# Performance work log

Measured on AMD Instinct MI355X. Metric: run time of the kernel, lower is better.

Reference implementation:

```python
import jax, jax.numpy as jnp
import numpy as np

N = 50000      # nodes
E = 400000     # edges (avg degree 8)
F_IN = 128     # input feature dim
H = 4          # heads (layer 1)
D = 128        # hidden per head
C = 3          # classes (layer 2 out, 1 head)
EPS = 1e-5     # BatchNorm eps
SLOPE = 0.2    # LeakyReLU negative slope (DGL GATConv default)


def setup_inputs() -> dict:
    key = jax.random.key(0)
    ks = jax.random.split(key, 16)
    s = jnp.float32(0.05)
    return {
        "features": jax.random.normal(ks[0], (N, F_IN), jnp.float32),
        "src": jax.random.randint(ks[1], (E,), 0, N, jnp.int32),
        "dst": jax.random.randint(ks[2], (E,), 0, N, jnp.int32),
        # GATConv layer 1 params
        "W1": jax.random.normal(ks[3], (F_IN, H * D), jnp.float32) * s,
        "al1": jax.random.normal(ks[4], (H, D), jnp.float32) * s,
        "ar1": jax.random.normal(ks[5], (H, D), jnp.float32) * s,
        "b1": jnp.zeros((H * D,), jnp.float32),
        "Wres1": jax.random.normal(ks[6], (F_IN, H * D), jnp.float32) * s,
        # BatchNorm1d (inference mode)
        "bn_gamma": jnp.ones((H * D,), jnp.float32),
        "bn_beta": jnp.zeros((H * D,), jnp.float32),
        "bn_mean": jnp.zeros((H * D,), jnp.float32),
        "bn_var": jnp.ones((H * D,), jnp.float32),
        # GATConv layer 2 params (1 head, C out)
        "W2": jax.random.normal(ks[7], (H * D, C), jnp.float32) * s,
        "al2": jax.random.normal(ks[8], (1, C), jnp.float32) * s,
        "ar2": jax.random.normal(ks[9], (1, C), jnp.float32) * s,
        "b2": jnp.zeros((C,), jnp.float32),
        "Wres2": jax.random.normal(ks[10], (H * D, C), jnp.float32) * s,
    }


def _gat_layer(x, src, dst, W, attn_l, attn_r, bias, Wres, heads, dim):
    """DGL GATConv (eval mode): gather, LeakyReLU score, segment softmax,
    weighted scatter-sum, linear residual, bias."""
    n = x.shape[0]
    z = (x @ W).reshape(n, heads, dim)                 # [N,H,D]
    el = jnp.sum(z * attn_l, axis=-1)                  # [N,H]
    er = jnp.sum(z * attn_r, axis=-1)                  # [N,H]
    e = jax.nn.leaky_relu(el[src] + er[dst], SLOPE)    # [E,H]
    # segment softmax over incoming edges of each dst node
    m = jax.ops.segment_max(e, dst, num_segments=n)    # [N,H]
    ex = jnp.exp(e - m[dst])                           # [E,H]
    den = jax.ops.segment_sum(ex, dst, num_segments=n) # [N,H]
    alpha = ex / den[dst]                              # [E,H]
    # weighted message aggregation
    rst = jax.ops.segment_sum(z[src] * alpha[..., None], dst, num_segments=n)  # [N,H,D]
    res = (x @ Wres).reshape(n, heads, dim)
    return rst + res + bias.reshape(1, heads, dim)


def reference(features, src, dst, W1, al1, ar1, b1, Wres1,
              bn_gamma, bn_beta, bn_mean, bn_var,
              W2, al2, ar2, b2, Wres2):
    h = _gat_layer(features, src, dst, W1, al1, ar1, b1, Wres1, H, D)
    h = h.reshape(N, H * D)
    # BatchNorm1d (inference) + ELU; dropout is identity in eval mode
    h = (h - bn_mean) * jax.lax.rsqrt(bn_var + EPS) * bn_gamma + bn_beta
    h = jax.nn.elu(h)
    h = _gat_layer(h, src, dst, W2, al2, ar2, b2, Wres2, 1, C)
    return h[:, 0, :]  # squeeze head dim -> [N, C]
```

## Files before the change

### kernel.cpp

```cpp
#include <hip/hip_runtime.h>
#include <hip/hip_bf16.h>

#define N_NODES 50000
#define N_EDGES 400000
#define FIN     128
#define HD      512
#define SLOPE   0.2f
#define NB_X    782

typedef __hip_bfloat16 bf16;
typedef __bf16 bf16x8 __attribute__((ext_vector_type(8)));
typedef __bf16 bf16x4 __attribute__((ext_vector_type(4)));
typedef __bf16 bf16x2 __attribute__((ext_vector_type(2)));
typedef float  f32x4  __attribute__((ext_vector_type(4)));
typedef float  f32x2  __attribute__((ext_vector_type(2)));

__global__ void sentinel_k(float* out, int n) {
    int i = blockIdx.x * 256 + threadIdx.x;
    if (i < n) out[i] = 12288.0f;
}

__global__ __launch_bounds__(256) void prep_k(const float* __restrict__ W1, const float* __restrict__ Wres1,
                                              const float* __restrict__ al1, const float* __restrict__ ar1,
                                              const float* __restrict__ W2, const float* __restrict__ Wres2,
                                              const float* __restrict__ b1,
                                              const float* __restrict__ bnm, const float* __restrict__ bnv,
                                              const float* __restrict__ bng, const float* __restrict__ bnb,
                                              bf16* __restrict__ Wfrag, float* __restrict__ tab,
                                              bf16* __restrict__ wlrb,
                                              int* __restrict__ deg, int* __restrict__ cur0) {
    int b = blockIdx.x;
    if (b < 196) {
        int i = b * 256 + threadIdx.x;
        if (i < N_NODES) { deg[i] = 0; cur0[i] = 0; }
        return;
    }
    b -= 196;
    if (b < 64) {
        int f = b * 256 + threadIdx.x;
        int lane = f & 63, unit = f >> 6;
        int tile = unit >> 3, ks = unit & 7;
        int cl = lane & 15, rg = lane >> 4;
        int gc = tile * 16 + cl;
        int k0 = ks * 32 + rg * 8;
        bf16x8 v;
#pragma unroll
        for (int j = 0; j < 8; ++j) {
            int kk = k0 + j;
            float x = (kk < 128) ? W1[kk * HD + gc] : Wres1[(kk - 128) * HD + gc];
            v[j] = (__bf16)x;
        }
        *reinterpret_cast<bf16x8*>(reinterpret_cast<char*>(Wfrag) + (size_t)f * 16) = v;
        return;
    }
    b -= 64;
    if (b < 16) {
        int i = b * 256 + threadIdx.x;
        int gc = i >> 3, c = i & 7;
        float v;
        if (c < 2) {
            float rs = rsqrtf(bnv[gc] + 1e-5f) * bng[gc];
            v = (c == 0) ? rs : (b1[gc] - bnm[gc]) * rs + bnb[gc];
        } else if (c < 5) {
            v = W2[gc * 3 + (c - 2)];
        } else {
            v = Wres2[gc * 3 + (c - 5)];
        }
        tab[i] = v;
        return;
    }
    for (int i = 0; i < 8; ++i) {
        int e = i * 256 + threadIdx.x;
        int ks = e >> 9, lane = (e >> 3) & 63, j = e & 7;
        int r = lane & 15, rg = lane >> 4;
        int k = ks * 32 + rg * 8 + j;
        float v = 0.f;
        if (r < 4) {
            for (int d = 0; d < 128; ++d) v += W1[k * HD + r * 128 + d] * al1[r * 128 + d];
        } else if (r < 8) {
            int h = r - 4;
            for (int d = 0; d < 128; ++d) v += W1[k * HD + h * 128 + d] * ar1[h * 128 + d];
        }
        wlrb[e] = __float2bfloat16(v);
    }
}

__global__ __launch_bounds__(256) void eler_k(const float* __restrict__ X,
                                              const bf16* __restrict__ wlrb,
                                              float* __restrict__ el, float* __restrict__ er,
                                              bf16* __restrict__ Xb,
                                              const int* __restrict__ dst, int* __restrict__ deg) {
    if (blockIdx.x >= NB_X) {
        int e = (blockIdx.x - NB_X) * 256 + threadIdx.x;
        if (e < N_EDGES) atomicAdd(&deg[dst[e]], 1);
        return;
    }
    __shared__ __align__(16) char XSb[64 * 256];
    const int t = threadIdx.x;
    const int w = t >> 6, lane = t & 63;
    const int cl = lane & 15, rg = lane >> 4;
    const int m0 = blockIdx.x * 64;

#pragma unroll
    for (int j = 0; j < 8; ++j) {
        int e = j * 1024 + t * 4;
        int row = e >> 7, col = e & 127;
        int grow = m0 + row;
        int gc = grow < N_NODES ? grow : N_NODES - 1;
        f32x4 v = *reinterpret_cast<const f32x4*>(X + (size_t)gc * FIN + col);
        bf16x4 bv = {(__bf16)v[0], (__bf16)v[1], (__bf16)v[2], (__bf16)v[3]};
        if (grow < N_NODES)
            *reinterpret_cast<bf16x4*>(Xb + (size_t)grow * FIN + col) = bv;
        int byte = (row * 256 + col * 2) ^ ((row & 7) << 4);
        *reinterpret_cast<bf16x4*>(XSb + byte) = bv;
    }
    __syncthreads();

    f32x4 a = {0.f, 0.f, 0.f, 0.f};
    const int row = w * 16 + cl;
    const int swz = (row & 7) << 4;
#pragma unroll
    for (int ks = 0; ks < 4; ++ks) {
        bf16x8 af = *reinterpret_cast<const bf16x8*>(
            reinterpret_cast<const char*>(wlrb) + ((size_t)(ks * 64 + lane)) * 16);
        int byte = (row * 256 + ks * 64 + rg * 16) ^ swz;
        bf16x8 bf = *reinterpret_cast<const bf16x8*>(XSb + byte);
        a = __builtin_amdgcn_mfma_f32_16x16x32_bf16(af, bf, a, 0, 0, 0);
    }
    int n = m0 + row;
    if (n < N_NODES) {
        if (rg == 0)      *reinterpret_cast<float4*>(el + (size_t)n * 4) = make_float4(a[0], a[1], a[2], a[3]);
        else if (rg == 1) *reinterpret_cast<float4*>(er + (size_t)n * 4) = make_float4(a[0], a[1], a[2], a[3]);
    }
}

__global__ __launch_bounds__(256) void scan1_k(const int* __restrict__ deg,
                                               int* __restrict__ rloc, int* __restrict__ blksum) {
    __shared__ int wsum[4];
    int t = threadIdx.x, b = blockIdx.x;
    int i = b * 256 + t;
    int v = (i < N_NODES) ? deg[i] : 0;
    int lane = t & 63, w = t >> 6;
    int x = v;
#pragma unroll
    for (int off = 1; off < 64; off <<= 1) {
        int y = __shfl_up(x, off);
        if (lane >= off) x += y;
    }
    if (lane == 63) wsum[w] = x;
    __syncthreads();
    int wadd = 0;
    if (w > 0) wadd += wsum[0];
    if (w > 1) wadd += wsum[1];
    if (w > 2) wadd += wsum[2];
    int incl = x + wadd;
    if (i < N_NODES) rloc[i] = incl - v;
    if (t == 255) blksum[b] = incl;
}

__global__ __launch_bounds__(256) void scan2_k(int* __restrict__ blksum) {
    __shared__ int wsum[4];
    int t = threadIdx.x;
    int v = (t < 196) ? blksum[t] : 0;
    int lane = t & 63, w = t >> 6;
    int x = v;
#pragma unroll
    for (int off = 1; off < 64; off <<= 1) {
        int y = __shfl_up(x, off);
        if (lane >= off) x += y;
    }
    if (lane == 63) wsum[w] = x;
    __syncthreads();
    int wadd = 0;
    if (w > 0) wadd += wsum[0];
    if (w > 1) wadd += wsum[1];
    if (w > 2) wadd += wsum[2];
    if (t < 196) blksum[t] = x + wadd - v;
}

__global__ void fill_k(const int* __restrict__ src, const int* __restrict__ dst,
                       const int* __restrict__ rloc, const int* __restrict__ bsum,
                       int* __restrict__ cur0, int* __restrict__ csr) {
    int e = blockIdx.x * 256 + threadIdx.x;
    if (e < N_EDGES) {
        int d = dst[e];
        int slot = atomicAdd(&cur0[d], 1);
        csr[rloc[d] + bsum[d >> 8] + slot] = src[e];
    }
}

__global__ __launch_bounds__(1024) void aggX_k(const int* __restrict__ rloc, const int* __restrict__ bsum,
                                               const int* __restrict__ degA, const int* __restrict__ csr,
                                               const float* __restrict__ el, const float* __restrict__ er,
                                               const bf16* __restrict__ Xb, bf16* __restrict__ AGGb,
                                               float* __restrict__ den4) {
    const int w = threadIdx.x >> 6, lane = threadIdx.x & 63;
    const int sub = lane >> 5, ll = lane & 31;
    int n = blockIdx.x * 32 + w * 2 + sub;
    const bool valid = n < N_NODES;
    if (!valid) n = N_NODES - 1;
    const int beg = rloc[n] + bsum[n >> 8];
    const int deg = degA[n];
    const float4 ern = *reinterpret_cast<const float4*>(er + (size_t)n * 4);
    const char* Xbc = reinterpret_cast<const char*>(Xb);

    f32x2 accA[4] = {{0.f,0.f},{0.f,0.f},{0.f,0.f},{0.f,0.f}};
    f32x2 accB[4] = {{0.f,0.f},{0.f,0.f},{0.f,0.f},{0.f,0.f}};
    float4 dp = make_float4(0.f, 0.f, 0.f, 0.f);

    for (int base = 0; base < deg; base += 32) {
        const int cnt = min(32, deg - base);
        int s = 0;
        if (ll < cnt) s = csr[beg + base + ll];
        float4 e4 = *reinterpret_cast<const float4*>(el + (size_t)s * 4);
        float4 p; float e;
        e = e4.x + ern.x; e = e > 0.f ? e : SLOPE * e; p.x = __expf(e);
        e = e4.y + ern.y; e = e > 0.f ? e : SLOPE * e; p.y = __expf(e);
        e = e4.z + ern.z; e = e > 0.f ? e : SLOPE * e; p.z = __expf(e);
        e = e4.w + ern.w; e = e > 0.f ? e : SLOPE * e; p.w = __expf(e);

        for (int j = 0; j < cnt; ++j) {
            int idx = sub * 32 + j;
            int sj = __shfl(s, idx);
            uint2 xv = *reinterpret_cast<const uint2*>(Xbc + (size_t)sj * 256 + ll * 8);
            float4 pj;
            pj.x = __shfl(p.x, idx);
            pj.y = __shfl(p.y, idx);
            pj.z = __shfl(p.z, idx);
            pj.w = __shfl(p.w, idx);
            dp.x += pj.x; dp.y += pj.y; dp.z += pj.z; dp.w += pj.w;
            f32x2 xlo = {__uint_as_float(xv.x << 16), __uint_as_float(xv.x & 0xffff0000u)};
            f32x2 xhi = {__uint_as_float(xv.y << 16), __uint_as_float(xv.y & 0xffff0000u)};
            accA[0] += pj.x * xlo; accB[0] += pj.x * xhi;
            accA[1] += pj.y * xlo; accB[1] += pj.y * xhi;
            accA[2] += pj.z * xlo; accB[2] += pj.z * xhi;
            accA[3] += pj.w * xlo; accB[3] += pj.w * xhi;
        }
    }

    if (valid) {
#pragma unroll
        for (int h = 0; h < 4; ++h) {
            bf16x4 v = {(__bf16)accA[h][0], (__bf16)accA[h][1],
                        (__bf16)accB[h][0], (__bf16)accB[h][1]};
            *reinterpret_cast<bf16x4*>(AGGb + (size_t)n * 512 + h * 128 + ll * 4) = v;
        }
        if (ll == 0) *reinterpret_cast<float4*>(den4 + (size_t)n * 4) = dp;
    }
}

__global__ __launch_bounds__(256) void gemm2_k(
    const bf16* __restrict__ Xb, const bf16* __restrict__ AGGb,
    const float* __restrict__ den4,
    const bf16* __restrict__ Wfrag, const float* __restrict__ tab,
    const float* __restrict__ al2, const float* __restrict__ ar2,
    float* __restrict__ node2) {
    __shared__ __align__(16) char XS[32 * 256];
    __shared__ __align__(16) char AGS[32 * 1024];
    __shared__ float zsum[4][32][6];

    const int t = threadIdx.x;
    const int w = t >> 6, lane = t & 63;
    const int cl = lane & 15, rg = lane >> 4;
    const int m0 = blockIdx.x * 32;

#pragma unroll
    for (int j = 0; j < 2; ++j) {
        int L = j * 4096 + t * 16;
        int row = L >> 8, col = L & 255;
        int grow = m0 + row; grow = grow < N_NODES ? grow : N_NODES - 1;
        bf16x8 v = *reinterpret_cast<const bf16x8*>(
            reinterpret_cast<const char*>(Xb) + (size_t)grow * 256 + col);
        int byte = (row * 256 + col) ^ ((row & 7) << 4);
        *reinterpret_cast<bf16x8*>(XS + byte) = v;
    }
#pragma unroll
    for (int j = 0; j < 8; ++j) {
        int L = j * 4096 + t * 16;
        int row = L >> 10, col = L & 1023;
        int grow = m0 + row; grow = grow < N_NODES ? grow : N_NODES - 1;
        bf16x8 v = *reinterpret_cast<const bf16x8*>(
            reinterpret_cast<const char*>(AGGb) + (size_t)grow * 1024 + col);
        int byte = (row * 1024 + col) ^ ((row & 7) << 4);
        *reinterpret_cast<bf16x8*>(AGS + byte) = v;
    }
    __syncthreads();

    float invden[2];
#pragma unroll
    for (int mt = 0; mt < 2; ++mt) {
        int nn = m0 + mt * 16 + cl;
        nn = nn < N_NODES ? nn : N_NODES - 1;
        float d = den4[(size_t)nn * 4 + w];
        invden[mt] = d > 0.f ? 1.f / d : 0.f;
    }

    float z2p[2][3] = {}, r2p[2][3] = {};

#pragma unroll
    for (int ct = 0; ct < 8; ++ct) {
        const int unit = (w * 8 + ct) * 8;
        bf16x8 af[8];
#pragma unroll
        for (int ks = 0; ks < 8; ++ks)
            af[ks] = *reinterpret_cast<const bf16x8*>(
                reinterpret_cast<const char*>(Wfrag) + ((size_t)(unit + ks) * 64 + lane) * 16);
        const int gcl = w * 128 + ct * 16 + rg * 4;
        f32x4 t0[4], t1[4];
#pragma unroll
        for (int i = 0; i < 4; ++i) {
            t0[i] = *reinterpret_cast<const f32x4*>(tab + (size_t)(gcl + i) * 8);
            t1[i] = *reinterpret_cast<const f32x4*>(tab + (size_t)(gcl + i) * 8 + 4);
        }
#pragma unroll
        for (int mt = 0; mt < 2; ++mt) {
            int row = mt * 16 + cl;
            int swz = (row & 7) << 4;
            f32x4 aA = {0.f, 0.f, 0.f, 0.f};
            f32x4 aX = {0.f, 0.f, 0.f, 0.f};
#pragma unroll
            for (int ks = 0; ks < 4; ++ks) {
                int byte = (row * 1024 + w * 256 + ks * 64 + rg * 16) ^ swz;
                bf16x8 bfr = *reinterpret_cast<const bf16x8*>(AGS + byte);
                aA = __builtin_amdgcn_mfma_f32_16x16x32_bf16(af[ks], bfr, aA, 0, 0, 0);
            }
#pragma unroll
            for (int ks = 0; ks < 4; ++ks) {
                int byte = (row * 256 + ks * 64 + rg * 16) ^ swz;
                bf16x8 bfr = *reinterpret_cast<const bf16x8*>(XS + byte);
                aX = __builtin_amdgcn_mfma_f32_16x16x32_bf16(af[ks + 4], bfr, aX, 0, 0, 0);
            }
#pragma unroll
            for (int i = 0; i < 4; ++i) {
                float z = aA[i] * invden[mt] + aX[i];
                float hv = z * t0[i][0] + t0[i][1];
                hv = hv > 0.f ? hv : (__expf(hv) - 1.f);
                z2p[mt][0] += hv * t0[i][2]; z2p[mt][1] += hv * t0[i][3]; z2p[mt][2] += hv * t1[i][0];
                r2p[mt][0] += hv * t1[i][1]; r2p[mt][1] += hv * t1[i][2]; r2p[mt][2] += hv * t1[i][3];
            }
        }
    }

#pragma unroll
    for (int mt = 0; mt < 2; ++mt)
#pragma unroll
        for (int c = 0; c < 3; ++c) {
            z2p[mt][c] += __shfl_xor(z2p[mt][c], 16);
            z2p[mt][c] += __shfl_xor(z2p[mt][c], 32);
            r2p[mt][c] += __shfl_xor(r2p[mt][c], 16);
            r2p[mt][c] += __shfl_xor(r2p[mt][c], 32);
        }
    if (rg == 0) {
#pragma unroll
        for (int mt = 0; mt < 2; ++mt) {
            int nl = mt * 16 + cl;
            zsum[w][nl][0] = z2p[mt][0]; zsum[w][nl][1] = z2p[mt][1]; zsum[w][nl][2] = z2p[mt][2];
            zsum[w][nl][3] = r2p[mt][0]; zsum[w][nl][4] = r2p[mt][1]; zsum[w][nl][5] = r2p[mt][2];
        }
    }
    __syncthreads();
    if (t < 32) {
        float v[6];
#pragma unroll
        for (int c = 0; c < 6; ++c)
            v[c] = zsum[0][t][c] + zsum[1][t][c] + zsum[2][t][c] + zsum[3][t][c];
        int n = m0 + t;
        if (n < N_NODES) {
            float e2l = v[0] * al2[0] + v[1] * al2[1] + v[2] * al2[2];
            float e2r = v[0] * ar2[0] + v[1] * ar2[1] + v[2] * ar2[2];
            *reinterpret_cast<float4*>(node2 + (size_t)n * 8) = make_float4(v[0], v[1], v[2], e2l);
            *reinterpret_cast<float4*>(node2 + (size_t)n * 8 + 4) = make_float4(v[3], v[4], v[5], e2r);
        }
    }
}

__global__ __launch_bounds__(256) void agg2_k(const int* __restrict__ rloc, const int* __restrict__ bsum,
                                              const int* __restrict__ degA, const int* __restrict__ csr,
                                              const float* __restrict__ node2,
                                              const float* __restrict__ b2, float* __restrict__ out) {
    int wv = threadIdx.x >> 6, lane = threadIdx.x & 63;
    int n = blockIdx.x * 4 + wv;
    int beg = rloc[n] + bsum[n >> 8];
    int deg = degA[n];
    float ern = node2[(size_t)n * 8 + 7];
    float den = 0.f, a0 = 0.f, a1 = 0.f, a2 = 0.f;
    for (int j = lane; j < deg; j += 64) {
        int s = csr[beg + j];
        float4 v = *reinterpret_cast<const float4*>(node2 + (size_t)s * 8);
        float e = v.w + ern;
        e = e > 0.f ? e : SLOPE * e;
        float p = __expf(e);
        den += p;
        a0 += p * v.x; a1 += p * v.y; a2 += p * v.z;
    }
#pragma unroll
    for (int off = 32; off > 0; off >>= 1) {
        den += __shfl_xor(den, off);
        a0 += __shfl_xor(a0, off); a1 += __shfl_xor(a1, off); a2 += __shfl_xor(a2, off);
    }
    if (lane == 0) {
        float inv = deg > 0 ? 1.f / den : 0.f;
        float4 r = *reinterpret_cast<const float4*>(node2 + (size_t)n * 8 + 4);
        out[(size_t)n * 3 + 0] = a0 * inv + r.x + b2[0];
        out[(size_t)n * 3 + 1] = a1 * inv + r.y + b2[1];
        out[(size_t)n * 3 + 2] = a2 * inv + r.z + b2[2];
    }
}

extern "C" void kernel_launch(void* const* d_in, const int* in_sizes, int n_in,
                              void* d_out, int out_size, void* d_ws, size_t ws_size,
                              hipStream_t stream) {
    const float* X     = (const float*)d_in[0];
    const int*   src   = (const int*)d_in[1];
    const int*   dst   = (const int*)d_in[2];
    const float* W1    = (const float*)d_in[3];
    const float* al1   = (const float*)d_in[4];
    const float* ar1   = (const float*)d_in[5];
    const float* b1    = (const float*)d_in[6];
    const float* Wres1 = (const float*)d_in[7];
    const float* bng   = (const float*)d_in[8];
    const float* bnb   = (const float*)d_in[9];
    const float* bnm   = (const float*)d_in[10];
    const float* bnv   = (const float*)d_in[11];
    const float* W2    = (const float*)d_in[12];
    const float* al2   = (const float*)d_in[13];
    const float* ar2   = (const float*)d_in[14];
    const float* b2    = (const float*)d_in[15];
    const float* Wres2 = (const float*)d_in[16];
    float* out = (float*)d_out;

    char* p = (char*)d_ws;
    auto carve = [&](size_t bytes) -> char* {
        char* r = p;
        p += (bytes + 255) & ~(size_t)255;
        return r;
    };
    bf16*  Wfrag  = (bf16*)carve((size_t)512 * 256 * 2);
    float* tab    = (float*)carve((size_t)512 * 8 * 4);
    bf16*  wlrb   = (bf16*)carve((size_t)2048 * 2);
    float* el     = (float*)carve((size_t)N_NODES * 4 * 4);
    float* er     = (float*)carve((size_t)N_NODES * 4 * 4);
    int*   deg    = (int*)carve((size_t)N_NODES * 4);
    int*   rloc   = (int*)carve((size_t)(N_NODES + 256) * 4);
    int*   cur0   = (int*)carve((size_t)N_NODES * 4);
    int*   bsum   = (int*)carve((size_t)256 * 4);
    int*   csr    = (int*)carve((size_t)N_EDGES * 4);
    bf16*  Xb     = (bf16*)carve((size_t)N_NODES * FIN * 2);
    bf16*  AGGb   = (bf16*)carve((size_t)N_NODES * 512 * 2);
    float* den4   = (float*)carve((size_t)(N_NODES + 64) * 4 * 4);
    float* node2  = (float*)carve((size_t)N_NODES * 8 * 4);
    size_t need = (size_t)(p - (char*)d_ws);
    if (need > ws_size) {
        sentinel_k<<<(out_size + 255) / 256, 256, 0, stream>>>(out, out_size);
        return;
    }

    prep_k<<<196 + 64 + 16 + 1, 256, 0, stream>>>(W1, Wres1, al1, ar1, W2, Wres2, b1,
                                                  bnm, bnv, bng, bnb, Wfrag, tab, wlrb, deg, cur0);
    eler_k<<<NB_X + (N_EDGES + 255) / 256, 256, 0, stream>>>(X, wlrb, el, er, Xb, dst, deg);
    scan1_k<<<196, 256, 0, stream>>>(deg, rloc, bsum);
    scan2_k<<<1, 256, 0, stream>>>(bsum);
    fill_k<<<(N_EDGES + 255) / 256, 256, 0, stream>>>(src, dst, rloc, bsum, cur0, csr);
    aggX_k<<<(N_NODES + 31) / 32, 1024, 0, stream>>>(rloc, bsum, deg, csr, el, er, Xb, AGGb, den4);
    gemm2_k<<<(N_NODES + 31) / 32, 256, 0, stream>>>(Xb, AGGb, den4, Wfrag, tab, al2, ar2, node2);
    agg2_k<<<N_NODES / 4, 256, 0, stream>>>(rloc, bsum, deg, csr, node2, b2, out);
}
```

Measured before the change: 176.6 us.

## Fuse neighbor aggregation into the GEMM kernel via shared memory

Merges the layer-1 neighbor aggregation kernel into the following GEMM kernel. Each 256-thread block now aggregates its 32 nodes in four passes and writes the bf16 aggregates and softmax denominators straight into shared memory, so the AGGb and den4 global buffers are no longer written and read back. This removes about 51 MB of global round-trip traffic and one launch. In exchange the aggregation runs with 256 threads per block instead of 1024, which lowers the latency hiding available for the irregular gathers, and the GEMM phase cannot start until a block's whole aggregation finishes.

After: 212.6 us. 20.4% more time.

```diff
diff --git a/kernel.cpp b/kernel.cpp
--- a/kernel.cpp
+++ b/kernel.cpp
@@ -189,109 +189,96 @@
     }
 }
 
-__global__ __launch_bounds__(1024) void aggX_k(const int* __restrict__ rloc, const int* __restrict__ bsum,
-                                               const int* __restrict__ degA, const int* __restrict__ csr,
-                                               const float* __restrict__ el, const float* __restrict__ er,
-                                               const bf16* __restrict__ Xb, bf16* __restrict__ AGGb,
-                                               float* __restrict__ den4) {
-    const int w = threadIdx.x >> 6, lane = threadIdx.x & 63;
-    const int sub = lane >> 5, ll = lane & 31;
-    int n = blockIdx.x * 32 + w * 2 + sub;
-    const bool valid = n < N_NODES;
-    if (!valid) n = N_NODES - 1;
-    const int beg = rloc[n] + bsum[n >> 8];
-    const int deg = degA[n];
-    const float4 ern = *reinterpret_cast<const float4*>(er + (size_t)n * 4);
-    const char* Xbc = reinterpret_cast<const char*>(Xb);
-
-    f32x2 accA[4] = {{0.f,0.f},{0.f,0.f},{0.f,0.f},{0.f,0.f}};
-    f32x2 accB[4] = {{0.f,0.f},{0.f,0.f},{0.f,0.f},{0.f,0.f}};
-    float4 dp = make_float4(0.f, 0.f, 0.f, 0.f);
-
-    for (int base = 0; base < deg; base += 32) {
-        const int cnt = min(32, deg - base);
-        int s = 0;
-        if (ll < cnt) s = csr[beg + base + ll];
-        float4 e4 = *reinterpret_cast<const float4*>(el + (size_t)s * 4);
-        float4 p; float e;
-        e = e4.x + ern.x; e = e > 0.f ? e : SLOPE * e; p.x = __expf(e);
-        e = e4.y + ern.y; e = e > 0.f ? e : SLOPE * e; p.y = __expf(e);
-        e = e4.z + ern.z; e = e > 0.f ? e : SLOPE * e; p.z = __expf(e);
-        e = e4.w + ern.w; e = e > 0.f ? e : SLOPE * e; p.w = __expf(e);
-
-        for (int j = 0; j < cnt; ++j) {
-            int idx = sub * 32 + j;
-            int sj = __shfl(s, idx);
-            uint2 xv = *reinterpret_cast<const uint2*>(Xbc + (size_t)sj * 256 + ll * 8);
-            float4 pj;
-            pj.x = __shfl(p.x, idx);
-            pj.y = __shfl(p.y, idx);
-            pj.z = __shfl(p.z, idx);
-            pj.w = __shfl(p.w, idx);
-            dp.x += pj.x; dp.y += pj.y; dp.z += pj.z; dp.w += pj.w;
-            f32x2 xlo = {__uint_as_float(xv.x << 16), __uint_as_float(xv.x & 0xffff0000u)};
-            f32x2 xhi = {__uint_as_float(xv.y << 16), __uint_as_float(xv.y & 0xffff0000u)};
-            accA[0] += pj.x * xlo; accB[0] += pj.x * xhi;
-            accA[1] += pj.y * xlo; accB[1] += pj.y * xhi;
-            accA[2] += pj.z * xlo; accB[2] += pj.z * xhi;
-            accA[3] += pj.w * xlo; accB[3] += pj.w * xhi;
-        }
-    }
-
-    if (valid) {
-#pragma unroll
-        for (int h = 0; h < 4; ++h) {
-            bf16x4 v = {(__bf16)accA[h][0], (__bf16)accA[h][1],
-                        (__bf16)accB[h][0], (__bf16)accB[h][1]};
-            *reinterpret_cast<bf16x4*>(AGGb + (size_t)n * 512 + h * 128 + ll * 4) = v;
-        }
-        if (ll == 0) *reinterpret_cast<float4*>(den4 + (size_t)n * 4) = dp;
-    }
-}
-
-__global__ __launch_bounds__(256) void gemm2_k(
-    const bf16* __restrict__ Xb, const bf16* __restrict__ AGGb,
-    const float* __restrict__ den4,
+__global__ __launch_bounds__(256) void fuse_k(
+    const int* __restrict__ rloc, const int* __restrict__ bsum,
+    const int* __restrict__ degA, const int* __restrict__ csr,
+    const float* __restrict__ el, const float* __restrict__ er,
+    const bf16* __restrict__ Xb,
     const bf16* __restrict__ Wfrag, const float* __restrict__ tab,
     const float* __restrict__ al2, const float* __restrict__ ar2,
     float* __restrict__ node2) {
     __shared__ __align__(16) char XS[32 * 256];
     __shared__ __align__(16) char AGS[32 * 1024];
+    __shared__ float dens[32][4];
     __shared__ float zsum[4][32][6];
 
     const int t = threadIdx.x;
     const int w = t >> 6, lane = t & 63;
+    const int sub = lane >> 5, ll = lane & 31;
     const int cl = lane & 15, rg = lane >> 4;
     const int m0 = blockIdx.x * 32;
+    const char* Xbc = reinterpret_cast<const char*>(Xb);
 
 #pragma unroll
     for (int j = 0; j < 2; ++j) {
         int L = j * 4096 + t * 16;
         int row = L >> 8, col = L & 255;
         int grow = m0 + row; grow = grow < N_NODES ? grow : N_NODES - 1;
-        bf16x8 v = *reinterpret_cast<const bf16x8*>(
-            reinterpret_cast<const char*>(Xb) + (size_t)grow * 256 + col);
+        bf16x8 v = *reinterpret_cast<const bf16x8*>(Xbc + (size_t)grow * 256 + col);
         int byte = (row * 256 + col) ^ ((row & 7) << 4);
         *reinterpret_cast<bf16x8*>(XS + byte) = v;
     }
-#pragma unroll
-    for (int j = 0; j < 8; ++j) {
-        int L = j * 4096 + t * 16;
-        int row = L >> 10, col = L & 1023;
-        int grow = m0 + row; grow = grow < N_NODES ? grow : N_NODES - 1;
-        bf16x8 v = *reinterpret_cast<const bf16x8*>(
-            reinterpret_cast<const char*>(AGGb) + (size_t)grow * 1024 + col);
-        int byte = (row * 1024 + col) ^ ((row & 7) << 4);
-        *reinterpret_cast<bf16x8*>(AGS + byte) = v;
+
+#pragma unroll
+    for (int pass = 0; pass < 4; ++pass) {
+        const int nl = pass * 8 + w * 2 + sub;
+        int n = m0 + nl;
+        const bool valid = n < N_NODES;
+        if (!valid) n = N_NODES - 1;
+        const int beg = rloc[n] + bsum[n >> 8];
+        const int deg = degA[n];
+        const float4 ern = *reinterpret_cast<const float4*>(er + (size_t)n * 4);
+
+        f32x2 accA[4] = {{0.f,0.f},{0.f,0.f},{0.f,0.f},{0.f,0.f}};
+        f32x2 accB[4] = {{0.f,0.f},{0.f,0.f},{0.f,0.f},{0.f,0.f}};
+        float4 dp = make_float4(0.f, 0.f, 0.f, 0.f);
+
+        for (int base = 0; base < deg; base += 32) {
+            const int cnt = min(32, deg - base);
+            int s = 0;
+            if (ll < cnt) s = csr[beg + base + ll];
+            float4 e4 = *reinterpret_cast<const float4*>(el + (size_t)s * 4);
+            float4 p; float e;
+            e = e4.x + ern.x; e = e > 0.f ? e : SLOPE * e; p.x = __expf(e);
+            e = e4.y + ern.y; e = e > 0.f ? e : SLOPE * e; p.y = __expf(e);
+            e = e4.z + ern.z; e = e > 0.f ? e : SLOPE * e; p.z = __expf(e);
+            e = e4.w + ern.w; e = e > 0.f ? e : SLOPE * e; p.w = __expf(e);
+
+            for (int j = 0; j < cnt; ++j) {
+                int idx = sub * 32 + j;
+                int sj = __shfl(s, idx);
+                uint2 xv = *reinterpret_cast<const uint2*>(Xbc + (size_t)sj * 256 + ll * 8);
+                float4 pj;
+                pj.x = __shfl(p.x, idx);
+                pj.y = __shfl(p.y, idx);
+                pj.z = __shfl(p.z, idx);
+                pj.w = __shfl(p.w, idx);
+                dp.x += pj.x; dp.y += pj.y; dp.z += pj.z; dp.w += pj.w;
+                f32x2 xlo = {__uint_as_float(xv.x << 16), __uint_as_float(xv.x & 0xffff0000u)};
+                f32x2 xhi = {__uint_as_float(xv.y << 16), __uint_as_float(xv.y & 0xffff0000u)};
+                accA[0] += pj.x * xlo; accB[0] += pj.x * xhi;
+                accA[1] += pj.y * xlo; accB[1] += pj.y * xhi;
+                accA[2] += pj.z * xlo; accB[2] += pj.z * xhi;
+                accA[3] += pj.w * xlo; accB[3] += pj.w * xhi;
+            }
+        }
+
+        const int swzr = (nl & 7) << 4;
+#pragma unroll
+        for (int h = 0; h < 4; ++h) {
+            bf16x4 v = {(__bf16)accA[h][0], (__bf16)accA[h][1],
+                        (__bf16)accB[h][0], (__bf16)accB[h][1]};
+            int byte = (nl * 1024 + h * 256 + ll * 8) ^ swzr;
+            *reinterpret_cast<bf16x4*>(AGS + byte) = v;
+        }
+        if (ll == 0) *reinterpret_cast<float4*>(&dens[nl][0]) = dp;
     }
     __syncthreads();
 
     float invden[2];
 #pragma unroll
     for (int mt = 0; mt < 2; ++mt) {
-        int nn = m0 + mt * 16 + cl;
-        nn = nn < N_NODES ? nn : N_NODES - 1;
-        float d = den4[(size_t)nn * 4 + w];
+        float d = dens[mt * 16 + cl][w];
         invden[mt] = d > 0.f ? 1.f / d : 0.f;
     }
 
@@ -446,8 +433,6 @@
     int*   bsum   = (int*)carve((size_t)256 * 4);
     int*   csr    = (int*)carve((size_t)N_EDGES * 4);
     bf16*  Xb     = (bf16*)carve((size_t)N_NODES * FIN * 2);
-    bf16*  AGGb   = (bf16*)carve((size_t)N_NODES * 512 * 2);
-    float* den4   = (float*)carve((size_t)(N_NODES + 64) * 4 * 4);
     float* node2  = (float*)carve((size_t)N_NODES * 8 * 4);
     size_t need = (size_t)(p - (char*)d_ws);
     if (need > ws_size) {
@@ -461,7 +446,7 @@
     scan1_k<<<196, 256, 0, stream>>>(deg, rloc, bsum);
     scan2_k<<<1, 256, 0, stream>>>(bsum);
     fill_k<<<(N_EDGES + 255) / 256, 256, 0, stream>>>(src, dst, rloc, bsum, cur0, csr);
-    aggX_k<<<(N_NODES + 31) / 32, 1024, 0, stream>>>(rloc, bsum, deg, csr, el, er, Xb, AGGb, den4);
-    gemm2_k<<<(N_NODES + 31) / 32, 256, 0, stream>>>(Xb, AGGb, den4, Wfrag, tab, al2, ar2, node2);
+    fuse_k<<<(N_NODES + 31) / 32, 256, 0, stream>>>(rloc, bsum, deg, csr, el, er, Xb,
+                                                    Wfrag, tab, al2, ar2, node2);
     agg2_k<<<N_NODES / 4, 256, 0, stream>>>(rloc, bsum, deg, csr, node2, b2, out);
 }
```
